# Optimization experiments

Measured on AMD Instinct MI355X. Metric: run time of the kernel, lower is better.

Reference implementation:

```python
import jax, jax.numpy as jnp
import numpy as np
from jax import lax

G, N0, E, P = 50, 1000, 4000, 10          # graphs, nodes/graph, edges/graph, patients
FEAT, NHID, GDIM, RATIO = 1036, 128, 32, 0.2
NLAYERS = 3


def setup_inputs():
    key = jax.random.key(0)
    ks = jax.random.split(key, 32)
    x = jax.random.uniform(ks[0], (G * N0, FEAT), jnp.float32)
    off = (jnp.arange(G) * N0)[:, None]
    src = jax.random.randint(ks[1], (G, E), 0, N0) + off
    dst = jax.random.randint(ks[2], (G, E), 0, N0) + off
    edge_index = jnp.stack([src.reshape(-1), dst.reshape(-1)]).astype(jnp.int32)
    graphs_per_pat = jnp.full((P,), G // P, jnp.int32)

    def lin(k, i, o):
        return jax.random.normal(k, (i, o), jnp.float32) / np.float32(np.sqrt(i))

    d = {"x": x, "edge_index": edge_index, "graphs_per_pat": graphs_per_pat}
    ins = [FEAT, NHID, NHID]
    ki = 3
    for l in range(NLAYERS):
        d[f"c{l}_wl"] = lin(ks[ki], ins[l], NHID)
        d[f"c{l}_bl"] = jnp.zeros(NHID, jnp.float32)
        d[f"c{l}_wr"] = lin(ks[ki + 1], ins[l], NHID)
        d[f"p{l}_wrel"] = lin(ks[ki + 2], NHID, 1)
        d[f"p{l}_brel"] = jnp.zeros(1, jnp.float32)
        d[f"p{l}_wroot"] = lin(ks[ki + 3], NHID, 1)
        ki += 4
    d["lin1_w"] = lin(ks[ki], 2 * NHID, NHID); d["lin1_b"] = jnp.zeros(NHID, jnp.float32)
    d["lin2_w"] = lin(ks[ki + 1], NHID, GDIM); d["lin2_b"] = jnp.zeros(GDIM, jnp.float32)
    d["grade_w"] = lin(ks[ki + 2], GDIM, 3); d["grade_b"] = jnp.zeros(3, jnp.float32)
    d["haz_w"] = lin(ks[ki + 3], GDIM, 1); d["haz_b"] = jnp.zeros(1, jnp.float32)
    return d


def _sage(x, src, dst, m, wl, bl, wr, M):
    # PyG SAGEConv, mean aggregation: out = lin_l(mean_j x_j) + lin_r(x_i)
    agg = jax.ops.segment_sum(x[src] * m[:, None], dst, num_segments=M)
    cnt = jax.ops.segment_sum(m, dst, num_segments=M)
    mean = agg / jnp.maximum(cnt, 1.0)[:, None]
    return mean @ wl + bl + x @ wr


def _sag_pool(x, src, dst, m, wrel, brel, wroot, n, k):
    # SAGPooling: GraphConv (add aggr) score -> per-graph top-k -> tanh gate -> edge filter
    M = G * n
    agg = jax.ops.segment_sum(x[src] * m[:, None], dst, num_segments=M)
    score = (agg @ wrel + brel + x @ wroot).reshape(G, n)  # [G, n]
    _, idx = lax.top_k(score, k)                            # [G, k]
    sel = jnp.take_along_axis(score, idx, axis=1)           # [G, k]
    perm = (idx + (jnp.arange(G) * n)[:, None]).reshape(-1)
    nx = x[perm] * jnp.tanh(sel).reshape(-1, 1)             # [G*k, NHID]
    mapping = jnp.full((M,), -1, jnp.int32).at[perm].set(jnp.arange(G * k, dtype=jnp.int32))
    ns, nd = mapping[src], mapping[dst]
    nm = m * (ns >= 0) * (nd >= 0)                          # keep edge iff both endpoints survive
    return nx, jnp.maximum(ns, 0), jnp.maximum(nd, 0), nm


def _forward(x, edge_index, graphs_per_pat, params):
    # normalize_graphs: first 12 feature columns divided by their column max
    x = jnp.concatenate([x[:, :12] / jnp.max(x[:, :12], axis=0, keepdims=True), x[:, 12:]], axis=1)
    src, dst = edge_index[0], edge_index[1]
    m = jnp.ones(src.shape[0], x.dtype)
    n = N0
    xs = []
    for l in range(NLAYERS):
        k = int(np.ceil(RATIO * n))
        x = jax.nn.relu(_sage(x, src, dst, m, params[f"c{l}_wl"], params[f"c{l}_bl"], params[f"c{l}_wr"], G * n))
        x, src, dst, m = _sag_pool(x, src, dst, m, params[f"p{l}_wrel"], params[f"p{l}_brel"], params[f"p{l}_wroot"], n, k)
        n = k
        xr = x.reshape(G, n, NHID)
        xs.append(jnp.concatenate([xr.max(axis=1), xr.mean(axis=1)], axis=1))  # [G, 2*NHID]
    h = xs[0] + xs[1] + xs[2]
    # patient-level mean pool
    bv = jnp.repeat(jnp.arange(P), graphs_per_pat, total_repeat_length=G)
    pooled = jax.ops.segment_sum(h, bv, num_segments=P) / graphs_per_pat[:, None].astype(h.dtype)
    h = jax.nn.relu(pooled @ params["lin1_w"] + params["lin1_b"])  # dropout omitted (deterministic ref)
    feats = jax.nn.relu(h @ params["lin2_w"] + params["lin2_b"])
    grade = jax.nn.log_softmax(feats @ params["grade_w"] + params["grade_b"], axis=1)
    hazard = jax.nn.sigmoid(feats @ params["haz_w"] + params["haz_b"]) * 6.0 - 3.0
    return feats, grade, hazard


def reference(x, edge_index, graphs_per_pat,
              c0_wl, c0_bl, c0_wr, p0_wrel, p0_brel, p0_wroot,
              c1_wl, c1_bl, c1_wr, p1_wrel, p1_brel, p1_wroot,
              c2_wl, c2_bl, c2_wr, p2_wrel, p2_brel, p2_wroot,
              lin1_w, lin1_b, lin2_w, lin2_b, grade_w, grade_b, haz_w, haz_b):
    params = dict(
        c0_wl=c0_wl, c0_bl=c0_bl, c0_wr=c0_wr, p0_wrel=p0_wrel, p0_brel=p0_brel, p0_wroot=p0_wroot,
        c1_wl=c1_wl, c1_bl=c1_bl, c1_wr=c1_wr, p1_wrel=p1_wrel, p1_brel=p1_brel, p1_wroot=p1_wroot,
        c2_wl=c2_wl, c2_bl=c2_bl, c2_wr=c2_wr, p2_wrel=p2_wrel, p2_brel=p2_brel, p2_wroot=p2_wroot,
        lin1_w=lin1_w, lin1_b=lin1_b, lin2_w=lin2_w, lin2_b=lin2_b,
        grade_w=grade_w, grade_b=grade_b, haz_w=haz_w, haz_b=haz_b)
    return _forward(x, edge_index, graphs_per_pat, params)
```

## Files before the change

kernel.cpp:

```cpp
#include <hip/hip_runtime.h>
#include <math.h>
#include <cfloat>

#define G_    50
#define N0_   1000
#define NEDGE 200000
#define EPG_  (NEDGE/G_)
#define P_    10
#define FEAT_ 1036
#define NHID_ 128
#define GDIM_ 32
#define K0_   200
#define K1_   40
#define K2_   8
#define M0_   (G_*N0_)
#define M1_   (G_*K0_)
#define M2_   (G_*K1_)

#define KPAD_ 1088
#define MPAD0_ 50048
#define MPAD1_ 10112
#define MPAD2_ 2048

typedef __attribute__((ext_vector_type(8))) short s16x8;
typedef __attribute__((ext_vector_type(4))) float f32x4;

__device__ __forceinline__ unsigned f2bf1(float f) {
  unsigned u = __float_as_uint(f);
  return (u + 0x7FFFu + ((u >> 16) & 1u)) >> 16;
}
__device__ __forceinline__ unsigned packbf(float a, float b) {
  return f2bf1(a) | (f2bf1(b) << 16);
}

__device__ __forceinline__ void gload_lds16(const void* g, void* l) {
  __builtin_amdgcn_global_load_lds((const __attribute__((address_space(1))) void*)g,
                                   (__attribute__((address_space(3))) void*)l, 16, 0, 0);
}


__global__ void colmax_kernel(const float* __restrict__ x, int* __restrict__ scale_i) {
  int tid = threadIdx.x, wave = tid >> 6, lane = tid & 63;
  float mx[12];
#pragma unroll
  for (int j = 0; j < 12; j++) mx[j] = 0.f;
  for (int r = blockIdx.x * 256 + tid; r < M0_; r += gridDim.x * 256) {
    const float4* p = (const float4*)(x + (size_t)r * FEAT_);
    float4 a = p[0], b = p[1], c = p[2];
    mx[0] = fmaxf(mx[0], a.x); mx[1] = fmaxf(mx[1], a.y);
    mx[2] = fmaxf(mx[2], a.z); mx[3] = fmaxf(mx[3], a.w);
    mx[4] = fmaxf(mx[4], b.x); mx[5] = fmaxf(mx[5], b.y);
    mx[6] = fmaxf(mx[6], b.z); mx[7] = fmaxf(mx[7], b.w);
    mx[8] = fmaxf(mx[8], c.x); mx[9] = fmaxf(mx[9], c.y);
    mx[10] = fmaxf(mx[10], c.z); mx[11] = fmaxf(mx[11], c.w);
  }
#pragma unroll
  for (int off = 32; off > 0; off >>= 1)
#pragma unroll
    for (int j = 0; j < 12; j++) mx[j] = fmaxf(mx[j], __shfl_down(mx[j], off));
  __shared__ float red[4][12];
  if (lane == 0)
#pragma unroll
    for (int j = 0; j < 12; j++) red[wave][j] = mx[j];
  __syncthreads();
  if (tid < 12) {
    float m = fmaxf(fmaxf(red[0][tid], red[1][tid]), fmaxf(red[2][tid], red[3][tid]));
    atomicMax(scale_i + tid, __float_as_int(m));
  }
}

__global__ void build_wt0_kernel(const float* __restrict__ wl, const float* __restrict__ wr,
                                 const int* __restrict__ scale_i, unsigned short* __restrict__ WT) {
  int idx = blockIdx.x * blockDim.x + threadIdx.x;
  if (idx >= 256 * KPAD_) return;
  int c = idx / KPAD_, j = idx % KPAD_;
  float w = 0.f;
  if (j < FEAT_) {
    w = (c < NHID_) ? wl[j * NHID_ + c] : wr[j * NHID_ + (c - NHID_)];
    if (j < 12) w *= 1.0f / __int_as_float(scale_i[j]);
  }
  WT[idx] = (unsigned short)f2bf1(w);
}

__global__ void build_wt12_kernel(const float* __restrict__ wl1, const float* __restrict__ wr1,
                                  const float* __restrict__ wl2, const float* __restrict__ wr2,
                                  unsigned short* __restrict__ WTA, unsigned short* __restrict__ WTB) {
  int idx = blockIdx.x * blockDim.x + threadIdx.x;
  if (idx >= 2 * 256 * 128) return;
  int l = idx >> 15, r = idx & 32767;
  int c = r >> 7, j = r & 127;
  const float* wl = l ? wl2 : wl1;
  const float* wr = l ? wr2 : wr1;
  float w = (c < NHID_) ? wl[j * NHID_ + c] : wr[j * NHID_ + (c - NHID_)];
  (l ? WTB : WTA)[r] = (unsigned short)f2bf1(w);
}

template <bool AF32>
__global__ __launch_bounds__(256) void mfma_gemm_kernel(const float* __restrict__ Af,
                                                        const unsigned short* __restrict__ Ab,
                                                        const unsigned short* __restrict__ WT,
                                                        float* __restrict__ C, int M,
                                                        int lda, int ldb, int kvalid, int ksteps) {
  __shared__ unsigned short As[2 * 128 * 32];
  __shared__ unsigned short Bs[2][2 * 256 * 32];
  const int bm = blockIdx.x * 128;
  const int tid = threadIdx.x, wave = tid >> 6, lane = tid & 63;
  const int wr = wave >> 1, wc = wave & 1;
  const int lhi = lane >> 4, llo = lane & 15;
  const int arow = tid >> 1, ahalf = tid & 1;
  f32x4 acc[4][8] = {};

  float fA[32];
  uint4 vA[4];

  auto loadA = [&](int st) {
    const int k0 = st * 64;
    int gr = bm + arow;
    int gk = k0 + ahalf * 32;
    if (AF32) {
      if (gr < M && gk + 32 <= kvalid) {
        const float4* ap = (const float4*)(Af + (size_t)gr * lda + gk);
#pragma unroll
        for (int j = 0; j < 8; j++) {
          float4 v = ap[j];
          fA[4 * j] = v.x; fA[4 * j + 1] = v.y; fA[4 * j + 2] = v.z; fA[4 * j + 3] = v.w;
        }
      } else {
        const float* ap = Af + (size_t)gr * lda + gk;
#pragma unroll
        for (int j = 0; j < 32; j++)
          fA[j] = (gr < M && gk + j < kvalid) ? ap[j] : 0.f;
      }
    } else {
      const uint4* ap = (const uint4*)(Ab + (size_t)gr * lda + gk);
#pragma unroll
      for (int j = 0; j < 4; j++) vA[j] = ap[j];
    }
  };
  auto writeA = [&]() {
    unsigned short* dstp = As + ahalf * 4096 + arow * 32;
    if (AF32) {
#pragma unroll
      for (int j = 0; j < 4; j++) {
        uint4 p;
        p.x = packbf(fA[8 * j + 0], fA[8 * j + 1]); p.y = packbf(fA[8 * j + 2], fA[8 * j + 3]);
        p.z = packbf(fA[8 * j + 4], fA[8 * j + 5]); p.w = packbf(fA[8 * j + 6], fA[8 * j + 7]);
        *(uint4*)(dstp + j * 8) = p;
      }
    } else {
#pragma unroll
      for (int j = 0; j < 4; j++) ((uint4*)dstp)[j] = vA[j];
    }
  };
  auto stageB = [&](int st, int b) {
    const int k0 = st * 64;
#pragma unroll
    for (int it = 0; it < 8; it++) {
      int c = it * 256 + wave * 64 + lane;
      int kk = c >> 10, r = (c >> 2) & 255, cb = c & 3;
      gload_lds16(WT + (size_t)r * ldb + k0 + kk * 32 + cb * 8, &Bs[b][(size_t)c * 8]);
    }
  };

  loadA(0);
  stageB(0, 0);
  writeA();
  __syncthreads();

  for (int st = 0; st < ksteps; st++) {
    const int bbuf = st & 1;
    const bool more = (st + 1 < ksteps);
    if (more) {
      loadA(st + 1);
      stageB(st + 1, bbuf ^ 1);
    }
#pragma unroll
    for (int kk = 0; kk < 2; kk++) {
      s16x8 a[4], b[8];
#pragma unroll
      for (int mt = 0; mt < 4; mt++)
        a[mt] = *(const s16x8*)&As[kk * 4096 + (wr * 64 + mt * 16 + llo) * 32 + lhi * 8];
#pragma unroll
      for (int nt = 0; nt < 8; nt++)
        b[nt] = *(const s16x8*)&Bs[bbuf][kk * 8192 + (wc * 128 + nt * 16 + llo) * 32 + lhi * 8];
#pragma unroll
      for (int mt = 0; mt < 4; mt++)
#pragma unroll
        for (int nt = 0; nt < 8; nt++)
          acc[mt][nt] = __builtin_amdgcn_mfma_f32_16x16x32_bf16(a[mt], b[nt], acc[mt][nt], 0, 0, 0);
    }
    if (more) {
      __syncthreads();
      writeA();
      __syncthreads();
    }
  }

#pragma unroll
  for (int mt = 0; mt < 4; mt++) {
#pragma unroll
    for (int q = 0; q < 4; q++) {
      int row = bm + wr * 64 + mt * 16 + lhi * 4 + q;
      if (row < M) {
#pragma unroll
        for (int nt = 0; nt < 8; nt++)
          C[(size_t)row * 256 + wc * 128 + nt * 16 + llo] = acc[mt][nt][q];
      }
    }
  }
}

__global__ __launch_bounds__(1024) void csr_graph_kernel(const int* __restrict__ src,
                                                         const int* __restrict__ dst,
                                                         int n,
                                                         int* __restrict__ deg,
                                                         int* __restrict__ offs,
                                                         int* __restrict__ eid) {
  __shared__ int sdeg[1024];
  __shared__ int soff[1024];
  __shared__ int scur[1024];
  __shared__ int spart[1024];
  const int g = blockIdx.x, tid = threadIdx.x;
  sdeg[tid] = 0;
  __syncthreads();
  const int e0 = g * EPG_;
  for (int e = tid; e < EPG_; e += 1024)
    atomicAdd(&sdeg[dst[e0 + e] - g * n], 1);
  __syncthreads();
  int v = (tid < n) ? sdeg[tid] : 0;
  spart[tid] = v;
  __syncthreads();
  for (int ofs = 1; ofs < 1024; ofs <<= 1) {
    int t = (tid >= ofs) ? spart[tid - ofs] : 0;
    __syncthreads();
    spart[tid] += t;
    __syncthreads();
  }
  if (tid < n) {
    soff[tid] = spart[tid] - sdeg[tid];
    scur[tid] = 0;
    deg[g * n + tid] = sdeg[tid];
    offs[g * n + tid] = g * EPG_ + soff[tid];
  }
  __syncthreads();
  for (int e = tid; e < EPG_; e += 1024) {
    int ge = e0 + e;
    int d = dst[ge] - g * n;
    int p = atomicAdd(&scur[d], 1);
    eid[g * EPG_ + soff[d] + p] = src[ge];
  }
}

__global__ void agg_sage_dots_kernel(const float* __restrict__ Y,
                                     const int* __restrict__ eid, const int* __restrict__ offs,
                                     const int* __restrict__ deg,
                                     const float* __restrict__ bl,
                                     const float* __restrict__ wrel, const float* __restrict__ wroot,
                                     float* __restrict__ X, float* __restrict__ T,
                                     float* __restrict__ R, int M) {
  int wid = threadIdx.x >> 6, lane = threadIdx.x & 63;
  int i = blockIdx.x * 4 + wid;
  if (i >= M) return;
  int d = deg[i], o = offs[i];
  float a0 = 0.f, a1 = 0.f;
  for (int j = 0; j < d; j++) {
    int s = eid[o + j];
    a0 += Y[(size_t)s * 256 + lane];
    a1 += Y[(size_t)s * 256 + 64 + lane];
  }
  float ic = 1.f / fmaxf((float)d, 1.f);
  float v0 = a0 * ic + bl[lane] + Y[(size_t)i * 256 + 128 + lane];
  float v1 = a1 * ic + bl[64 + lane] + Y[(size_t)i * 256 + 192 + lane];
  v0 = fmaxf(v0, 0.f); v1 = fmaxf(v1, 0.f);
  X[(size_t)i * 128 + lane] = v0;
  X[(size_t)i * 128 + 64 + lane] = v1;
  float t = v0 * wrel[lane] + v1 * wrel[64 + lane];
  float r = v0 * wroot[lane] + v1 * wroot[64 + lane];
#pragma unroll
  for (int off = 32; off > 0; off >>= 1) {
    t += __shfl_down(t, off);
    r += __shfl_down(r, off);
  }
  if (lane == 0) { T[i] = t; R[i] = r; }
}

template <int NP>
__global__ __launch_bounds__(1024) void pool_kernel(
    const float* __restrict__ X, const float* __restrict__ T, const float* __restrict__ R,
    const float* __restrict__ brel,
    const int* __restrict__ deg, const int* __restrict__ offs, const int* __restrict__ eid,
    int n, int k,
    unsigned short* __restrict__ NXB,
    int* __restrict__ degN, int* __restrict__ offsN, int* __restrict__ eidN,
    float* __restrict__ H) {
  __shared__ float val[NP];
  __shared__ int   ind[256];
  __shared__ int   lmap[NP];
  __shared__ float gate[256];
  __shared__ int   sdegN[256];
  __shared__ int   soffN[256];
  __shared__ float redmx[8][128];
  __shared__ float redsm[8][128];
  const int g = blockIdx.x, tid = threadIdx.x, nthr = blockDim.x;
  float b0 = brel[0];
  for (int i = tid; i < n; i += nthr) {
    int gi = g * n + i;
    int dd = deg[gi], o = offs[gi];
    float s = 0.f;
    for (int j = 0; j < dd; j++) s += T[eid[o + j]];
    val[i] = s + R[gi] + b0;
    lmap[i] = -1;
  }
  __syncthreads();
  for (int i = tid; i < n; i += nthr) {
    float vi = val[i];
    int rank = 0;
    for (int j = 0; j < n; j++) {
      float vj = val[j];
      rank += (vj > vi) || (vj == vi && j < i);
    }
    if (rank < k) {
      lmap[i] = rank;
      ind[rank] = i;
      gate[rank] = tanhf(vi);
    }
  }
  __syncthreads();
  for (int idx = tid; idx < k * 128; idx += nthr) {
    int t = idx >> 7, c = idx & 127;
    float v = X[(size_t)(g * n + ind[t]) * 128 + c] * gate[t];
    NXB[(size_t)(g * k + t) * 128 + c] = (unsigned short)f2bf1(v);
  }
  {
    int c = tid & 127, seg = tid >> 7;
    float mxv = -FLT_MAX, smv = 0.f;
    for (int t = seg; t < k; t += 8) {
      float v = X[(size_t)(g * n + ind[t]) * 128 + c] * gate[t];
      mxv = fmaxf(mxv, v);
      smv += v;
    }
    redmx[seg][c] = mxv;
    redsm[seg][c] = smv;
  }
  __syncthreads();
  if (tid < 128) {
    float Mv = redmx[0][tid], S = redsm[0][tid];
#pragma unroll
    for (int s2 = 1; s2 < 8; s2++) { Mv = fmaxf(Mv, redmx[s2][tid]); S += redsm[s2][tid]; }
    H[g * 256 + tid] += Mv;
    H[g * 256 + 128 + tid] += S / (float)k;
  }
  if (degN) {
    for (int t = tid; t < k; t += nthr) sdegN[t] = 0;
    __syncthreads();
    for (int d = tid; d < n; d += nthr) {
      int ld = lmap[d];
      if (ld < 0) continue;
      int gd = g * n + d, dd = deg[gd], o = offs[gd];
      int cnt = 0;
      for (int j = 0; j < dd; j++)
        cnt += (lmap[eid[o + j] - g * n] >= 0);
      sdegN[ld] = cnt;
    }
    __syncthreads();
    if (tid == 0) {
      int run = 0;
      for (int t = 0; t < k; t++) { soffN[t] = run; run += sdegN[t]; }
    }
    __syncthreads();
    for (int d = tid; d < n; d += nthr) {
      int ld = lmap[d];
      if (ld < 0) continue;
      int gd = g * n + d, dd = deg[gd], o = offs[gd];
      int p = 0;
      for (int j = 0; j < dd; j++) {
        int ls = lmap[eid[o + j] - g * n];
        if (ls >= 0) eidN[g * EPG_ + soffN[ld] + (p++)] = g * k + ls;
      }
      degN[g * k + ld] = p;
      offsN[g * k + ld] = g * EPG_ + soffN[ld];
    }
  }
}

__global__ void head_kernel(const float* __restrict__ H, const int* __restrict__ gpp,
                            const float* __restrict__ lin1_w, const float* __restrict__ lin1_b,
                            const float* __restrict__ lin2_w, const float* __restrict__ lin2_b,
                            const float* __restrict__ grade_w, const float* __restrict__ grade_b,
                            const float* __restrict__ haz_w, const float* __restrict__ haz_b,
                            float* __restrict__ out) {
  __shared__ float pooled[P_][256];
  __shared__ float h1[P_][NHID_];
  __shared__ float feats[P_][GDIM_];
  __shared__ int off[P_ + 1];
  int tid = threadIdx.x;
  if (tid == 0) {
    off[0] = 0;
    for (int p = 0; p < P_; p++) off[p + 1] = min(off[p] + gpp[p], G_);
  }
  __syncthreads();
  for (int idx = tid; idx < P_ * 256; idx += blockDim.x) {
    int p = idx >> 8, c = idx & 255;
    int a = off[p], b = (p == P_ - 1) ? G_ : off[p + 1];
    float s = 0.f;
    for (int gq = a; gq < b; gq++) s += H[gq * 256 + c];
    pooled[p][c] = s / (float)gpp[p];
  }
  __syncthreads();
  for (int idx = tid; idx < P_ * NHID_; idx += blockDim.x) {
    int p = idx >> 7, o = idx & 127;
    float acc = lin1_b[o];
    for (int c = 0; c < 256; c++) acc += pooled[p][c] * lin1_w[c * NHID_ + o];
    h1[p][o] = fmaxf(acc, 0.f);
  }
  __syncthreads();
  for (int idx = tid; idx < P_ * GDIM_; idx += blockDim.x) {
    int p = idx / GDIM_, o = idx % GDIM_;
    float acc = lin2_b[o];
    for (int c = 0; c < NHID_; c++) acc += h1[p][c] * lin2_w[c * GDIM_ + o];
    float f = fmaxf(acc, 0.f);
    feats[p][o] = f;
    out[p * GDIM_ + o] = f;
  }
  __syncthreads();
  if (tid < P_) {
    int p = tid;
    float l[3];
    float mx = -FLT_MAX;
    for (int j = 0; j < 3; j++) {
      float acc = grade_b[j];
      for (int c = 0; c < GDIM_; c++) acc += feats[p][c] * grade_w[c * 3 + j];
      l[j] = acc;
      mx = fmaxf(mx, acc);
    }
    float se = 0.f;
    for (int j = 0; j < 3; j++) se += expf(l[j] - mx);
    float lse = mx + logf(se);
    for (int j = 0; j < 3; j++) out[P_ * GDIM_ + p * 3 + j] = l[j] - lse;
    float z = haz_b[0];
    for (int c = 0; c < GDIM_; c++) z += feats[p][c] * haz_w[c];
    out[P_ * GDIM_ + P_ * 3 + p] = 6.f / (1.f + expf(-z)) - 3.f;
  }
}

extern "C" void kernel_launch(void* const* d_in, const int* in_sizes, int n_in,
                              void* d_out, int out_size, void* d_ws, size_t ws_size,
                              hipStream_t stream) {
  (void)in_sizes; (void)n_in; (void)out_size; (void)ws_size;
  const float* x  = (const float*)d_in[0];
  const int* ei   = (const int*)d_in[1];
  const int* gpp  = (const int*)d_in[2];
  const float* c_wl[3]    = {(const float*)d_in[3],  (const float*)d_in[9],  (const float*)d_in[15]};
  const float* c_bl[3]    = {(const float*)d_in[4],  (const float*)d_in[10], (const float*)d_in[16]};
  const float* c_wr[3]    = {(const float*)d_in[5],  (const float*)d_in[11], (const float*)d_in[17]};
  const float* p_wrel[3]  = {(const float*)d_in[6],  (const float*)d_in[12], (const float*)d_in[18]};
  const float* p_brel[3]  = {(const float*)d_in[7],  (const float*)d_in[13], (const float*)d_in[19]};
  const float* p_wroot[3] = {(const float*)d_in[8],  (const float*)d_in[14], (const float*)d_in[20]};
  const float* lin1_w = (const float*)d_in[21];
  const float* lin1_b = (const float*)d_in[22];
  const float* lin2_w = (const float*)d_in[23];
  const float* lin2_b = (const float*)d_in[24];
  const float* grade_w = (const float*)d_in[25];
  const float* grade_b = (const float*)d_in[26];
  const float* haz_w = (const float*)d_in[27];
  const float* haz_b = (const float*)d_in[28];

  char* wsb = (char*)d_ws;
  size_t off = 0;
  auto alloc = [&](size_t bytes) -> void* {
    void* p = wsb + off;
    off += (bytes + 255) & ~(size_t)255;
    return p;
  };
  int*            SCALE = (int*)alloc(64 * 4);
  unsigned short* WT0   = (unsigned short*)alloc((size_t)256 * KPAD_ * 2);
  unsigned short* WT1   = (unsigned short*)alloc((size_t)256 * 128 * 2);
  unsigned short* WT2   = (unsigned short*)alloc((size_t)256 * 128 * 2);
  float*          YZ    = (float*)alloc((size_t)M0_ * 256 * 4);
  float*          H     = (float*)alloc((size_t)G_ * 256 * 4);
  float* X     = (float*)alloc((size_t)M0_ * 128 * 4);
  unsigned short* NXB = (unsigned short*)alloc((size_t)MPAD1_ * 128 * 2);
  float* T     = (float*)alloc((size_t)M0_ * 4);
  float* R     = (float*)alloc((size_t)M0_ * 4);
  int*   DEG0  = (int*)alloc((size_t)M0_ * 4);
  int*   OFF0  = (int*)alloc((size_t)M0_ * 4);
  int*   EID0  = (int*)alloc((size_t)NEDGE * 4);
  int*   DEG1  = (int*)alloc((size_t)M1_ * 4);
  int*   OFF1  = (int*)alloc((size_t)M1_ * 4);
  int*   EID1  = (int*)alloc((size_t)NEDGE * 4);

  const int* src0 = ei;
  const int* dst0 = ei + NEDGE;

  hipMemsetAsync(H, 0, G_ * 256 * sizeof(float), stream);
  hipMemsetAsync(SCALE, 0, 12 * sizeof(int), stream);

  colmax_kernel<<<128, 256, 0, stream>>>(x, SCALE);
  build_wt0_kernel<<<(256 * KPAD_ + 255) / 256, 256, 0, stream>>>(c_wl[0], c_wr[0], SCALE, WT0);
  build_wt12_kernel<<<(2 * 256 * 128 + 255) / 256, 256, 0, stream>>>(c_wl[1], c_wr[1], c_wl[2], c_wr[2], WT1, WT2);

  csr_graph_kernel<<<G_, 1024, 0, stream>>>(src0, dst0, N0_, DEG0, OFF0, EID0);
  mfma_gemm_kernel<true><<<MPAD0_ / 128, 256, 0, stream>>>(x, nullptr, WT0, YZ, M0_, FEAT_, KPAD_, FEAT_, KPAD_ / 64);
  agg_sage_dots_kernel<<<(M0_ + 3) / 4, 256, 0, stream>>>(YZ, EID0, OFF0, DEG0, c_bl[0], p_wrel[0], p_wroot[0], X, T, R, M0_);
  pool_kernel<1024><<<G_, 1024, 0, stream>>>(X, T, R, p_brel[0], DEG0, OFF0, EID0,
                                             N0_, K0_, NXB, DEG1, OFF1, EID1, H);

  mfma_gemm_kernel<false><<<MPAD1_ / 128, 256, 0, stream>>>(nullptr, NXB, WT1, YZ, M1_, 128, 128, 128, 2);
  agg_sage_dots_kernel<<<(M1_ + 3) / 4, 256, 0, stream>>>(YZ, EID1, OFF1, DEG1, c_bl[1], p_wrel[1], p_wroot[1], X, T, R, M1_);
  pool_kernel<256><<<G_, 1024, 0, stream>>>(X, T, R, p_brel[1], DEG1, OFF1, EID1,
                                            K0_, K1_, NXB, DEG0, OFF0, EID0, H);

  mfma_gemm_kernel<false><<<MPAD2_ / 128, 256, 0, stream>>>(nullptr, NXB, WT2, YZ, M2_, 128, 128, 128, 2);
  agg_sage_dots_kernel<<<(M2_ + 3) / 4, 256, 0, stream>>>(YZ, EID0, OFF0, DEG0, c_bl[2], p_wrel[2], p_wroot[2], X, T, R, M2_);
  pool_kernel<64><<<G_, 1024, 0, stream>>>(X, T, R, p_brel[2], DEG0, OFF0, EID0,
                                           K1_, K2_, NXB, nullptr, nullptr, nullptr, H);

  head_kernel<<<1, 256, 0, stream>>>(H, gpp, lin1_w, lin1_b, lin2_w, lin2_b,
                                     grade_w, grade_b, haz_w, haz_b, (float*)d_out);
}
```

Baseline: 335.3 us.

## Replace rank-count top-k with bitonic sort and single-buffer the GEMM staging

The pool kernel's O(n^2) rank-counting top-k selection is replaced by an in-shared-memory bitonic sort over a power-of-two padded array. The aim is to cut the quadratic comparison work for the 1000-node first pooling layer. Separately, the MFMA GEMM drops its double-buffered register prefetch of A and B and now loads each k-step synchronously into a single LDS buffer. That lowers shared-memory and register use but gives up the overlap of global loads with compute. The bitonic sort does not break ties by index, so selection order for equal scores may differ from the original.

```diff
diff --git a/kernel.cpp b/kernel.cpp
--- a/kernel.cpp
+++ b/kernel.cpp
@@ -102,7 +102,7 @@
                                                         float* __restrict__ C, int M,
                                                         int lda, int ldb, int kvalid, int ksteps) {
   __shared__ unsigned short As[2 * 128 * 32];
-  __shared__ unsigned short Bs[2][2 * 256 * 32];
+  __shared__ unsigned short Bs[2 * 256 * 32];
   const int bm = blockIdx.x * 128;
   const int tid = threadIdx.x, wave = tid >> 6, lane = tid & 63;
   const int wr = wave >> 1, wc = wave & 1;
@@ -110,70 +110,48 @@
   const int arow = tid >> 1, ahalf = tid & 1;
   f32x4 acc[4][8] = {};
 
-  float fA[32];
-  uint4 vA[4];
-
-  auto loadA = [&](int st) {
-    const int k0 = st * 64;
-    int gr = bm + arow;
-    int gk = k0 + ahalf * 32;
-    if (AF32) {
-      if (gr < M && gk + 32 <= kvalid) {
-        const float4* ap = (const float4*)(Af + (size_t)gr * lda + gk);
-#pragma unroll
-        for (int j = 0; j < 8; j++) {
-          float4 v = ap[j];
-          fA[4 * j] = v.x; fA[4 * j + 1] = v.y; fA[4 * j + 2] = v.z; fA[4 * j + 3] = v.w;
-        }
-      } else {
-        const float* ap = Af + (size_t)gr * lda + gk;
-#pragma unroll
-        for (int j = 0; j < 32; j++)
-          fA[j] = (gr < M && gk + j < kvalid) ? ap[j] : 0.f;
-      }
-    } else {
-      const uint4* ap = (const uint4*)(Ab + (size_t)gr * lda + gk);
-#pragma unroll
-      for (int j = 0; j < 4; j++) vA[j] = ap[j];
-    }
-  };
-  auto writeA = [&]() {
-    unsigned short* dstp = As + ahalf * 4096 + arow * 32;
-    if (AF32) {
-#pragma unroll
-      for (int j = 0; j < 4; j++) {
-        uint4 p;
-        p.x = packbf(fA[8 * j + 0], fA[8 * j + 1]); p.y = packbf(fA[8 * j + 2], fA[8 * j + 3]);
-        p.z = packbf(fA[8 * j + 4], fA[8 * j + 5]); p.w = packbf(fA[8 * j + 6], fA[8 * j + 7]);
-        *(uint4*)(dstp + j * 8) = p;
-      }
-    } else {
-#pragma unroll
-      for (int j = 0; j < 4; j++) ((uint4*)dstp)[j] = vA[j];
-    }
-  };
-  auto stageB = [&](int st, int b) {
+  for (int st = 0; st < ksteps; st++) {
     const int k0 = st * 64;
 #pragma unroll
     for (int it = 0; it < 8; it++) {
       int c = it * 256 + wave * 64 + lane;
       int kk = c >> 10, r = (c >> 2) & 255, cb = c & 3;
-      gload_lds16(WT + (size_t)r * ldb + k0 + kk * 32 + cb * 8, &Bs[b][(size_t)c * 8]);
-    }
-  };
-
-  loadA(0);
-  stageB(0, 0);
-  writeA();
-  __syncthreads();
-
-  for (int st = 0; st < ksteps; st++) {
-    const int bbuf = st & 1;
-    const bool more = (st + 1 < ksteps);
-    if (more) {
-      loadA(st + 1);
-      stageB(st + 1, bbuf ^ 1);
-    }
+      gload_lds16(WT + (size_t)r * ldb + k0 + kk * 32 + cb * 8, Bs + (size_t)c * 8);
+    }
+    {
+      int gr = bm + arow;
+      int gk = k0 + ahalf * 32;
+      unsigned short* dstp = As + ahalf * 4096 + arow * 32;
+      if (AF32) {
+        float f[32];
+        if (gr < M && gk + 32 <= kvalid) {
+          const float4* ap = (const float4*)(Af + (size_t)gr * lda + gk);
+#pragma unroll
+          for (int j = 0; j < 8; j++) {
+            float4 v = ap[j];
+            f[4 * j] = v.x; f[4 * j + 1] = v.y; f[4 * j + 2] = v.z; f[4 * j + 3] = v.w;
+          }
+        } else {
+          const float* ap = Af + (size_t)gr * lda + gk;
+#pragma unroll
+          for (int j = 0; j < 32; j++)
+            f[j] = (gr < M && gk + j < kvalid) ? ap[j] : 0.f;
+        }
+#pragma unroll
+        for (int j = 0; j < 4; j++) {
+          uint4 p;
+          p.x = packbf(f[8 * j + 0], f[8 * j + 1]); p.y = packbf(f[8 * j + 2], f[8 * j + 3]);
+          p.z = packbf(f[8 * j + 4], f[8 * j + 5]); p.w = packbf(f[8 * j + 6], f[8 * j + 7]);
+          *(uint4*)(dstp + j * 8) = p;
+        }
+      } else {
+        const uint4* ap = (const uint4*)(Ab + (size_t)gr * lda + gk);
+#pragma unroll
+        for (int j = 0; j < 4; j++) ((uint4*)dstp)[j] = ap[j];
+      }
+    }
+    __syncthreads();
+
 #pragma unroll
     for (int kk = 0; kk < 2; kk++) {
       s16x8 a[4], b[8];
@@ -182,18 +160,14 @@
         a[mt] = *(const s16x8*)&As[kk * 4096 + (wr * 64 + mt * 16 + llo) * 32 + lhi * 8];
 #pragma unroll
       for (int nt = 0; nt < 8; nt++)
-        b[nt] = *(const s16x8*)&Bs[bbuf][kk * 8192 + (wc * 128 + nt * 16 + llo) * 32 + lhi * 8];
+        b[nt] = *(const s16x8*)&Bs[kk * 8192 + (wc * 128 + nt * 16 + llo) * 32 + lhi * 8];
 #pragma unroll
       for (int mt = 0; mt < 4; mt++)
 #pragma unroll
         for (int nt = 0; nt < 8; nt++)
           acc[mt][nt] = __builtin_amdgcn_mfma_f32_16x16x32_bf16(a[mt], b[nt], acc[mt][nt], 0, 0, 0);
     }
-    if (more) {
-      __syncthreads();
-      writeA();
-      __syncthreads();
-    }
+    __syncthreads();
   }
 
 #pragma unroll
@@ -294,7 +268,7 @@
     int* __restrict__ degN, int* __restrict__ offsN, int* __restrict__ eidN,
     float* __restrict__ H) {
   __shared__ float val[NP];
-  __shared__ int   ind[256];
+  __shared__ int   ind[NP];
   __shared__ int   lmap[NP];
   __shared__ float gate[256];
   __shared__ int   sdegN[256];
@@ -303,27 +277,39 @@
   __shared__ float redsm[8][128];
   const int g = blockIdx.x, tid = threadIdx.x, nthr = blockDim.x;
   float b0 = brel[0];
-  for (int i = tid; i < n; i += nthr) {
-    int gi = g * n + i;
-    int dd = deg[gi], o = offs[gi];
-    float s = 0.f;
-    for (int j = 0; j < dd; j++) s += T[eid[o + j]];
-    val[i] = s + R[gi] + b0;
+  for (int i = tid; i < NP; i += nthr) {
     lmap[i] = -1;
-  }
-  __syncthreads();
-  for (int i = tid; i < n; i += nthr) {
-    float vi = val[i];
-    int rank = 0;
-    for (int j = 0; j < n; j++) {
-      float vj = val[j];
-      rank += (vj > vi) || (vj == vi && j < i);
-    }
-    if (rank < k) {
-      lmap[i] = rank;
-      ind[rank] = i;
-      gate[rank] = tanhf(vi);
-    }
+    float v = -FLT_MAX;
+    if (i < n) {
+      int gi = g * n + i;
+      int dd = deg[gi], o = offs[gi];
+      float s = 0.f;
+      for (int j = 0; j < dd; j++) s += T[eid[o + j]];
+      v = s + R[gi] + b0;
+    }
+    val[i] = v;
+    ind[i] = i;
+  }
+  __syncthreads();
+  for (int kk = 2; kk <= NP; kk <<= 1) {
+    for (int j = kk >> 1; j > 0; j >>= 1) {
+      for (int i = tid; i < NP; i += nthr) {
+        int ixj = i ^ j;
+        if (ixj > i) {
+          bool desc = ((i & kk) == 0);
+          float vi = val[i], vj = val[ixj];
+          if (desc ? (vi < vj) : (vi > vj)) {
+            val[i] = vj; val[ixj] = vi;
+            int tmp = ind[i]; ind[i] = ind[ixj]; ind[ixj] = tmp;
+          }
+        }
+      }
+      __syncthreads();
+    }
+  }
+  for (int t = tid; t < k; t += nthr) {
+    lmap[ind[t]] = t;
+    gate[t] = tanhf(val[t]);
   }
   __syncthreads();
   for (int idx = tid; idx < k * 128; idx += nthr) {
```

After: 271.9 us, median of 2. -18.9%, faster.
